# Optimization experiments

Measured on AMD Instinct MI355X. Metric: run time of the kernel, lower is better.

Reference implementation:

```python
import jax, jax.numpy as jnp
import numpy as np

B, T, V, WD = 32, 2048, 50000, 300        # batch, max_doc_len, batch vocab, word_dim
P, L, ND = 150, 7, 2                      # total patterns, max_pattern_length, num_diags
BIAS_SCALE = 1.0
ZERO = -100.0                             # max-plus semiring zero (repo: neg_infinity = -100*ones)
# end state per pattern = pattern_length - 1, for pattern_specs {5:50, 6:50, 7:50}
END_STATES = np.concatenate([np.full(50, 4), np.full(50, 5), np.full(50, 6)]).astype(np.int32)


def setup_inputs() -> dict:
    key = jax.random.key(0)
    ks = jax.random.split(key, 10)
    diags = jax.random.normal(ks[0], (P * ND * L, WD), jnp.float32)
    diags = diags / jnp.linalg.norm(diags, axis=1, keepdims=True)  # normalize() in __init__
    return {
        "embeddings_matrix": jax.random.normal(ks[1], (WD, V), jnp.float32),
        "diags": diags,
        "bias": jax.random.normal(ks[2], (P * ND * L, 1), jnp.float32),
        "epsilon": jax.random.normal(ks[3], (P, L - 1), jnp.float32),
        "mlp_w0": jax.random.normal(ks[4], (P, 100), jnp.float32) * 0.1,
        "mlp_b0": jnp.zeros((100,), jnp.float32),
        "mlp_w1": jax.random.normal(ks[5], (100, 2), jnp.float32) * 0.1,
        "mlp_b1": jnp.zeros((2,), jnp.float32),
        "docs": jax.random.randint(ks[6], (B, T), 0, V),
        "doc_lens": jax.random.randint(ks[7], (B,), 5, T + 1),
    }


def reference(embeddings_matrix, diags, bias, epsilon, mlp_w0, mlp_b0, mlp_w1, mlp_b1, docs, doc_lens):
    # Max-plus semiring: from_float = identity, times = +, plus = max, one = 0, zero = -100.
    # Transition scores for every token in the batch vocabulary: [V, P*ND*L]
    trans = (diags @ embeddings_matrix + BIAS_SCALE * bias).T
    # Gather per doc token, reshape, time-major: [T, B, P, ND, L]
    tm = trans[docs].reshape(B, T, P, ND, L).transpose(1, 0, 2, 3, 4)

    end_states = jnp.asarray(END_STATES)               # [P]
    active = jnp.arange(T)[:, None] < doc_lens[None, :]  # [T, B]

    zero_pad = jnp.full((B, P, 1), ZERO, trans.dtype)
    restart_pad = jnp.zeros((B, P, 1), trans.dtype)      # semiring one
    hid0 = jnp.full((B, P, L), ZERO, trans.dtype).at[:, :, 0].set(0.0)
    scores0 = jnp.full((B, P), ZERO, trans.dtype)
    eps_val = epsilon                                    # epsilon_scale = semiring one (=0) -> identity

    def step(carry, xs):
        hid, sc = carry
        tmat, act = xs  # tmat: [B, P, ND, L], act: [B]
        # epsilon transitions (shift by one state, additive in max-plus)
        after_eps = jnp.maximum(hid, jnp.concatenate([zero_pad, hid[:, :, :-1] + eps_val], axis=2))
        # main-path transitions (diag index -1), with restart padding at state 0
        main = jnp.concatenate([restart_pad, after_eps[:, :, :-1] + tmat[:, :, -1, :-1]], axis=2)
        # self loops (diag index 0); self_loop_scale = semiring one = 0
        self_loop = hid + tmat[:, :, 0, :]
        hid = jnp.maximum(main, self_loop)
        end_vals = jnp.take_along_axis(hid, end_states[None, :, None], axis=2)[:, :, 0]  # [B, P]
        sc = jnp.where(act[:, None], jnp.maximum(sc, end_vals), sc)
        return (hid, sc), None

    (_, scores), _ = jax.lax.scan(step, (hid0, scores0), (tm, active))
    # MLP head: Linear -> relu -> Linear
    h = scores @ mlp_w0 + mlp_b0
    return jax.nn.relu(h) @ mlp_w1 + mlp_b1
```

## Files before the change

kernel.cpp:

```cpp
#include <hip/hip_runtime.h>
#include <stdint.h>

#define B_   32
#define T_   2048
#define V_   50000
#define WD_  300
#define P_   150
#define KP   320
#define MP   2112
#define MB2  2176
#define NPAD 50048
#define CHUNK 64
#define NCH   32
#define NEGC (-1.0e30f)
#define VT_  391
#define MT_  17
#define NWG  6647

#define WS_EMBT      0u
#define WS_DIAGSB    32030720u
#define WS_TRANS     33423360u
#define WS_CHUNKOUT  0u
#define WS_NEEDED    244623360u

typedef __attribute__((ext_vector_type(8))) short bf16x8;
typedef __attribute__((ext_vector_type(4))) float f32x4;

#define GLOAD_LDS16(gp, lp) __builtin_amdgcn_global_load_lds( \
    (__attribute__((address_space(1))) void*)(gp), \
    (__attribute__((address_space(3))) void*)(lp), 16, 0, 0)

__device__ __forceinline__ unsigned short f2bf(float f){
  unsigned u = __builtin_bit_cast(unsigned, f);
  u = u + 0x7fffu + ((u >> 16) & 1u);
  return (unsigned short)(u >> 16);
}
__device__ __forceinline__ float bf_lo(unsigned u){ return __builtin_bit_cast(float, u << 16); }
__device__ __forceinline__ float bf_hi(unsigned u){ return __builtin_bit_cast(float, u & 0xffff0000u); }

__global__ __launch_bounds__(256) void k_transpose_emb(const float* __restrict__ emb,
                                                       unsigned short* __restrict__ embT){
  __shared__ float tile[32][65];
  int v0 = blockIdx.x * 64, k0 = blockIdx.y * 32;
  int tid = threadIdx.x;
  #pragma unroll
  for (int it = 0; it < 8; ++it){
    int idx = it * 256 + tid;
    int kk = idx >> 6, vv = idx & 63;
    int k = k0 + kk, v = v0 + vv;
    float val = 0.f;
    if (k < WD_ && v < V_) val = emb[(size_t)k * V_ + v];
    tile[kk][vv] = val;
  }
  __syncthreads();
  int row = tid >> 2, c = tid & 3;
  unsigned short e[8];
  #pragma unroll
  for (int i = 0; i < 8; ++i) e[i] = f2bf(tile[c*8 + i][row]);
  uint4 pk;
  pk.x = (unsigned)e[0] | ((unsigned)e[1] << 16);
  pk.y = (unsigned)e[2] | ((unsigned)e[3] << 16);
  pk.z = (unsigned)e[4] | ((unsigned)e[5] << 16);
  pk.w = (unsigned)e[6] | ((unsigned)e[7] << 16);
  *(uint4*)&embT[(size_t)(v0 + row) * KP + k0 + c*8] = pk;
}

__global__ __launch_bounds__(256) void k_conv_diags(const float* __restrict__ diags,
                                                    unsigned short* __restrict__ diagsB){
  int gid = blockIdx.x * 256 + threadIdx.x;
  int m = gid / 80;
  int k4 = (gid % 80) * 4;
  unsigned short e[4];
  #pragma unroll
  for (int i = 0; i < 4; ++i){
    int k = k4 + i;
    float v = (m < 2100 && k < WD_) ? diags[m * WD_ + k] : 0.f;
    e[i] = f2bf(v);
  }
  uint2 pk;
  pk.x = (unsigned)e[0] | ((unsigned)e[1] << 16);
  pk.y = (unsigned)e[2] | ((unsigned)e[3] << 16);
  *(uint2*)&diagsB[(size_t)m * KP + k4] = pk;
}

__global__ __launch_bounds__(256, 4) void k_gemm(const unsigned short* __restrict__ embT,
                                                 const unsigned short* __restrict__ diagsB,
                                                 const float* __restrict__ bias,
                                                 unsigned short* __restrict__ trans){
  __shared__ char smem[33792];
  int orig = blockIdx.x;
  int xcd = orig & 7, bidx = orig >> 3;
  int wg = (xcd < 7 ? xcd * 831 : 5817 + (xcd - 7) * 830) + bidx;
  int vt = wg / MT_, mt = wg - vt * MT_;
  int v0 = vt * 128, m0 = mt * 128;

  int tid = threadIdx.x;
  int w = tid >> 6, l = tid & 63;
  int wv = w & 1, wm = w >> 1;
  int lrow = l & 15, lq = l >> 4;

  f32x4 acc[4][4];
  #pragma unroll
  for (int i = 0; i < 4; ++i)
    #pragma unroll
    for (int j = 0; j < 4; ++j)
      acc[i][j] = (f32x4){0.f, 0.f, 0.f, 0.f};

  auto STAGE = [&](int buf, int kt){
    int k0 = kt * 32;
    char* bA = smem + buf * 16384;
    char* bB = bA + 8192;
    #pragma unroll
    for (int it = 0; it < 2; ++it){
      int idx = it * 256 + tid;
      int row = idx >> 2, slot = idx & 3;
      int sc = slot ^ ((row >> 1) & 3);
      GLOAD_LDS16(&embT[(size_t)(v0 + row) * KP + k0 + sc * 8], bA + idx * 16);
      GLOAD_LDS16(&diagsB[(size_t)(m0 + row) * KP + k0 + sc * 8], bB + idx * 16);
    }
  };

  STAGE(0, 0);
  #pragma unroll
  for (int kt = 0; kt < 10; ++kt){
    if (kt < 9){
      STAGE((kt + 1) & 1, kt + 1);
      asm volatile("s_waitcnt vmcnt(4)" ::: "memory");
    } else {
      asm volatile("s_waitcnt vmcnt(0)" ::: "memory");
    }
    __builtin_amdgcn_s_barrier();
    __builtin_amdgcn_sched_barrier(0);
    char* bA = smem + (kt & 1) * 16384;
    char* bB = bA + 8192;
    bf16x8 af[4], bg[4];
    #pragma unroll
    for (int i = 0; i < 4; ++i){
      int row = wv * 64 + i * 16 + lrow;
      af[i] = *(const bf16x8*)(bA + row * 64 + (lq ^ ((row >> 1) & 3)) * 16);
    }
    #pragma unroll
    for (int j = 0; j < 4; ++j){
      int row = wm * 64 + j * 16 + lrow;
      bg[j] = *(const bf16x8*)(bB + row * 64 + (lq ^ ((row >> 1) & 3)) * 16);
    }
    #pragma unroll
    for (int i = 0; i < 4; ++i)
      #pragma unroll
      for (int j = 0; j < 4; ++j)
        acc[i][j] = __builtin_amdgcn_mfma_f32_16x16x32_bf16(af[i], bg[j], acc[i][j], 0, 0, 0);
    __builtin_amdgcn_sched_barrier(0);
    __builtin_amdgcn_s_barrier();
  }

  float bv4[4];
  #pragma unroll
  for (int j = 0; j < 4; ++j){
    int mg = m0 + wm * 64 + j * 16 + lrow;
    bv4[j] = (mg < 2100) ? bias[mg] : 0.f;
  }
  unsigned short* eb = (unsigned short*)smem;
  #pragma unroll
  for (int i = 0; i < 4; ++i)
    #pragma unroll
    for (int j = 0; j < 4; ++j)
      #pragma unroll
      for (int r = 0; r < 4; ++r){
        int row = wv * 64 + i * 16 + lq * 4 + r;
        int col = wm * 64 + j * 16 + lrow;
        eb[row * 132 + col] = f2bf(acc[i][j][r] + bv4[j]);
      }
  __syncthreads();
  #pragma unroll
  for (int it = 0; it < 16; ++it){
    int idx2 = it * 256 + tid;
    int row = idx2 >> 5, ch = idx2 & 31;
    int vg = v0 + row, mg = m0 + ch * 4;
    if (vg < V_ && mg < MP){
      uint2 val = *(const uint2*)(smem + row * 264 + ch * 8);
      *(uint2*)&trans[(size_t)vg * MP + mg] = val;
    }
  }
}

__global__ __launch_bounds__(192) void k_scan(const unsigned short* __restrict__ trans,
                                              const int* __restrict__ docs,
                                              const int* __restrict__ doc_lens,
                                              const float* __restrict__ epsilon,
                                              float* __restrict__ chunkout){
  __shared__ int sdocs[CHUNK];
  int b = blockIdx.x >> 5, ch = blockIdx.x & 31;
  int tid = threadIdx.x;
  if (tid < CHUNK) sdocs[tid] = docs[b * T_ + ch * CHUNK + tid];
  __syncthreads();
  int p = tid;
  if (p >= P_) return;
  int doclen = doc_lens[b];
  float eps_r[6];
  #pragma unroll
  for (int i = 0; i < 6; ++i) eps_r[i] = epsilon[p*6 + i];
  int endsel = p / 50;

  float col[7][7], bvec[7], uvec[7], w;
  #pragma unroll
  for (int j = 0; j < 7; ++j)
    #pragma unroll
    for (int l = 0; l < 7; ++l) col[j][l] = (j == l) ? 0.f : NEGC;
  #pragma unroll
  for (int l = 0; l < 7; ++l){ bvec[l] = NEGC; uvec[l] = NEGC; }
  w = NEGC;

  const char* transB = (const char*)trans;

  auto LOADQ = [&](unsigned* q, int s){
    int idx = s < 63 ? s : 63;
    const unsigned* rp = (const unsigned*)(transB + (size_t)sdocs[idx] * (MP*2) + p*28);
    #pragma unroll
    for (int i = 0; i < 7; ++i) q[i] = rp[i];
  };

  auto step = [&](const unsigned* q, bool act){
    float tsf[7], tmn[6];
    tsf[0]=bf_lo(q[0]); tsf[1]=bf_hi(q[0]);
    tsf[2]=bf_lo(q[1]); tsf[3]=bf_hi(q[1]);
    tsf[4]=bf_lo(q[2]); tsf[5]=bf_hi(q[2]);
    tsf[6]=bf_lo(q[3]); tmn[0]=bf_hi(q[3]);
    tmn[1]=bf_lo(q[4]); tmn[2]=bf_hi(q[4]);
    tmn[3]=bf_lo(q[5]); tmn[4]=bf_hi(q[5]);
    tmn[5]=bf_lo(q[6]);
    #pragma unroll
    for (int j = 0; j < 7; ++j){
      #pragma unroll
      for (int l = 6; l >= 1; --l){
        if (l < j) continue;
        if (l == j){ col[j][l] = col[j][l] + tsf[l]; continue; }
        float ae;
        if (l - 1 == j) ae = col[j][l-1];
        else ae = fmaxf(col[j][l-1], col[j][l-2] + eps_r[l-2]);
        col[j][l] = fmaxf(ae + tmn[l-1], col[j][l] + tsf[l]);
      }
      if (j == 0) col[0][0] += tsf[0];
    }
    #pragma unroll
    for (int l = 6; l >= 1; --l){
      float ae;
      if (l == 1) ae = fmaxf(bvec[0], -100.0f);
      else ae = fmaxf(bvec[l-1], bvec[l-2] + eps_r[l-2]);
      bvec[l] = fmaxf(ae + tmn[l-1], bvec[l] + tsf[l]);
    }
    bvec[0] = fmaxf(0.0f, bvec[0] + tsf[0]);
    if (act){
      #pragma unroll
      for (int j = 0; j < 7; ++j){
        float c4 = (j <= 4) ? col[j][4] : NEGC;
        float c5 = (j <= 5) ? col[j][5] : NEGC;
        float c6 = col[j][6];
        float ce = (endsel == 0) ? c4 : ((endsel == 1) ? c5 : c6);
        uvec[j] = fmaxf(uvec[j], ce);
      }
      float be = (endsel == 0) ? bvec[4] : ((endsel == 1) ? bvec[5] : bvec[6]);
      w = fmaxf(w, be);
    }
  };

  unsigned q0[7], q1[7], q2[7], q3[7];
  LOADQ(q0, 0); LOADQ(q1, 1); LOADQ(q2, 2);
  int tbase = ch * CHUNK;
  for (int s = 0; s < CHUNK; s += 4){
    LOADQ(q3, s + 3); step(q0, (tbase + s)     < doclen);
    LOADQ(q0, s + 4); step(q1, (tbase + s + 1) < doclen);
    LOADQ(q1, s + 5); step(q2, (tbase + s + 2) < doclen);
    LOADQ(q2, s + 6); step(q3, (tbase + s + 3) < doclen);
  }

  float out[44];
  int idx = 0;
  #pragma unroll
  for (int j = 0; j < 7; ++j)
    #pragma unroll
    for (int l = j; l < 7; ++l) out[idx++] = col[j][l];
  #pragma unroll
  for (int l = 0; l < 7; ++l) out[28 + l] = bvec[l];
  #pragma unroll
  for (int l = 0; l < 7; ++l) out[35 + l] = uvec[l];
  out[42] = w; out[43] = 0.f;
  float* dst = chunkout + ((size_t)(b * NCH + ch) * P_ + p) * 44;
  #pragma unroll
  for (int i = 0; i < 11; ++i){
    float4 t2 = make_float4(out[4*i], out[4*i+1], out[4*i+2], out[4*i+3]);
    ((float4*)dst)[i] = t2;
  }
}

__global__ __launch_bounds__(192) void k_combine_mlp(const float* __restrict__ chunkout,
                                                     const float* __restrict__ w0,
                                                     const float* __restrict__ b0,
                                                     const float* __restrict__ w1,
                                                     const float* __restrict__ b1,
                                                     float* __restrict__ out){
  __shared__ float ssc[P_];
  __shared__ float sh[100];
  int b = blockIdx.x, tid = threadIdx.x;
  if (tid < P_){
    int p = tid;
    float h[7] = {0.f, -100.f, -100.f, -100.f, -100.f, -100.f, -100.f};
    float sc = -100.f;
    for (int ch = 0; ch < NCH; ++ch){
      const float* rec = chunkout + ((size_t)(b * NCH + ch) * P_ + p) * 44;
      float r[44];
      #pragma unroll
      for (int i = 0; i < 11; ++i){
        float4 t = ((const float4*)rec)[i];
        r[4*i] = t.x; r[4*i+1] = t.y; r[4*i+2] = t.z; r[4*i+3] = t.w;
      }
      #pragma unroll
      for (int j = 0; j < 7; ++j) sc = fmaxf(sc, r[35 + j] + h[j]);
      sc = fmaxf(sc, r[42]);
      constexpr int off[7] = {0, 7, 13, 18, 22, 25, 27};
      float nh[7];
      #pragma unroll
      for (int l = 0; l < 7; ++l){
        float v = r[28 + l];
        #pragma unroll
        for (int j = 0; j < 7; ++j){
          if (j <= l) v = fmaxf(v, r[off[j] + (l - j)] + h[j]);
        }
        nh[l] = v;
      }
      #pragma unroll
      for (int l = 0; l < 7; ++l) h[l] = nh[l];
    }
    ssc[p] = sc;
  }
  __syncthreads();
  if (tid < 100){
    float a = b0[tid];
    for (int pp = 0; pp < P_; ++pp) a += ssc[pp] * w0[pp * 100 + tid];
    sh[tid] = fmaxf(a, 0.f);
  }
  __syncthreads();
  if (tid < 2){
    float o = b1[tid];
    for (int j = 0; j < 100; ++j) o += sh[j] * w1[j * 2 + tid];
    out[b * 2 + tid] = o;
  }
}

extern "C" void kernel_launch(void* const* d_in, const int* in_sizes, int n_in,
                              void* d_out, int out_size, void* d_ws, size_t ws_size,
                              hipStream_t stream){
  const float* emb   = (const float*)d_in[0];
  const float* diags = (const float*)d_in[1];
  const float* bias  = (const float*)d_in[2];
  const float* eps   = (const float*)d_in[3];
  const float* w0    = (const float*)d_in[4];
  const float* b0    = (const float*)d_in[5];
  const float* w1    = (const float*)d_in[6];
  const float* b1    = (const float*)d_in[7];
  const int* docs    = (const int*)d_in[8];
  const int* dlens   = (const int*)d_in[9];

  if (ws_size < (size_t)WS_NEEDED) return;

  char* ws = (char*)d_ws;
  unsigned short* embT   = (unsigned short*)(ws + WS_EMBT);
  unsigned short* diagsB = (unsigned short*)(ws + WS_DIAGSB);
  unsigned short* trans  = (unsigned short*)(ws + WS_TRANS);
  float* chunkout        = (float*)(ws + WS_CHUNKOUT);
  float* outp = (float*)d_out;

  k_transpose_emb<<<dim3(NPAD/64, KP/32), 256, 0, stream>>>(emb, embT);
  k_conv_diags<<<(MB2*80 + 255)/256, 256, 0, stream>>>(diags, diagsB);
  k_gemm<<<NWG, 256, 0, stream>>>(embT, diagsB, bias, trans);
  k_scan<<<B_ * NCH, 192, 0, stream>>>(trans, docs, dlens, eps, chunkout);
  k_combine_mlp<<<B_, 192, 0, stream>>>(chunkout, w0, b0, w1, b1, outp);
}
```

Measured before the change: 220.7 us.

## Enlarge GEMM tile to 256x128, skip inactive scan chunks, use smaller chunks

The GEMM now uses 512-thread workgroups with a 256-row vocab tile, so each diags tile is reused across twice as many rows and the workgroup count is halved. The epilogue is split into two halves to fit LDS. The scan exits early for chunks entirely past doc_len, and the combine kernel stops at the last active chunk. When the workspace is large enough, 32-token chunks are used to expose more parallelism. The costs are higher register and LDS pressure per workgroup, lower occupancy, and an extra epilogue barrier.

After: 622.5 us. 182% more time.

```diff
diff --git a/kernel.cpp b/kernel.cpp
--- a/kernel.cpp
+++ b/kernel.cpp
@@ -9,19 +9,17 @@
 #define KP   320
 #define MP   2112
 #define MB2  2176
-#define NPAD 50048
-#define CHUNK 64
-#define NCH   32
+#define NPAD2 50176
+#define VT2  196
+#define MT_  17
+#define NWG2 3332
 #define NEGC (-1.0e30f)
-#define VT_  391
-#define MT_  17
-#define NWG  6647
-
-#define WS_EMBT      0u
-#define WS_DIAGSB    32030720u
-#define WS_TRANS     33423360u
-#define WS_CHUNKOUT  0u
-#define WS_NEEDED    244623360u
+
+#define WS_DIAGSB      32112640u
+#define WS_TRANS_BIG   54067200u
+#define WS_TRANS_SMALL 33505280u
+#define WS_NEED_BIG    265267200u
+#define WS_NEED_SMALL  244705280u
 
 typedef __attribute__((ext_vector_type(8))) short bf16x8;
 typedef __attribute__((ext_vector_type(4))) float f32x4;
@@ -83,20 +81,20 @@
   *(uint2*)&diagsB[(size_t)m * KP + k4] = pk;
 }
 
-__global__ __launch_bounds__(256, 4) void k_gemm(const unsigned short* __restrict__ embT,
+__global__ __launch_bounds__(512, 6) void k_gemm(const unsigned short* __restrict__ embT,
                                                  const unsigned short* __restrict__ diagsB,
                                                  const float* __restrict__ bias,
                                                  unsigned short* __restrict__ trans){
-  __shared__ char smem[33792];
+  __shared__ char smem[49152];
   int orig = blockIdx.x;
   int xcd = orig & 7, bidx = orig >> 3;
-  int wg = (xcd < 7 ? xcd * 831 : 5817 + (xcd - 7) * 830) + bidx;
+  int wg = (xcd < 4 ? xcd * 417 : 1668 + (xcd - 4) * 416) + bidx;
   int vt = wg / MT_, mt = wg - vt * MT_;
-  int v0 = vt * 128, m0 = mt * 128;
+  int v0 = vt * 256, m0 = mt * 128;
 
   int tid = threadIdx.x;
   int w = tid >> 6, l = tid & 63;
-  int wv = w & 1, wm = w >> 1;
+  int wm = w & 1, wv = w >> 1;
   int lrow = l & 15, lq = l >> 4;
 
   f32x4 acc[4][4];
@@ -108,15 +106,19 @@
 
   auto STAGE = [&](int buf, int kt){
     int k0 = kt * 32;
-    char* bA = smem + buf * 16384;
-    char* bB = bA + 8192;
+    char* bA = smem + buf * 24576;
+    char* bB = bA + 16384;
     #pragma unroll
     for (int it = 0; it < 2; ++it){
-      int idx = it * 256 + tid;
+      int idx = it * 512 + tid;
       int row = idx >> 2, slot = idx & 3;
       int sc = slot ^ ((row >> 1) & 3);
       GLOAD_LDS16(&embT[(size_t)(v0 + row) * KP + k0 + sc * 8], bA + idx * 16);
-      GLOAD_LDS16(&diagsB[(size_t)(m0 + row) * KP + k0 + sc * 8], bB + idx * 16);
+    }
+    {
+      int row = tid >> 2, slot = tid & 3;
+      int sc = slot ^ ((row >> 1) & 3);
+      GLOAD_LDS16(&diagsB[(size_t)(m0 + row) * KP + k0 + sc * 8], bB + tid * 16);
     }
   };
 
@@ -125,14 +127,14 @@
   for (int kt = 0; kt < 10; ++kt){
     if (kt < 9){
       STAGE((kt + 1) & 1, kt + 1);
-      asm volatile("s_waitcnt vmcnt(4)" ::: "memory");
+      asm volatile("s_waitcnt vmcnt(3)" ::: "memory");
     } else {
       asm volatile("s_waitcnt vmcnt(0)" ::: "memory");
     }
     __builtin_amdgcn_s_barrier();
     __builtin_amdgcn_sched_barrier(0);
-    char* bA = smem + (kt & 1) * 16384;
-    char* bB = bA + 8192;
+    char* bA = smem + (kt & 1) * 24576;
+    char* bB = bA + 16384;
     bf16x8 af[4], bg[4];
     #pragma unroll
     for (int i = 0; i < 4; ++i){
@@ -161,41 +163,51 @@
   }
   unsigned short* eb = (unsigned short*)smem;
   #pragma unroll
-  for (int i = 0; i < 4; ++i)
-    #pragma unroll
-    for (int j = 0; j < 4; ++j)
-      #pragma unroll
-      for (int r = 0; r < 4; ++r){
-        int row = wv * 64 + i * 16 + lq * 4 + r;
-        int col = wm * 64 + j * 16 + lrow;
-        eb[row * 132 + col] = f2bf(acc[i][j][r] + bv4[j]);
-      }
-  __syncthreads();
-  #pragma unroll
-  for (int it = 0; it < 16; ++it){
-    int idx2 = it * 256 + tid;
-    int row = idx2 >> 5, ch = idx2 & 31;
-    int vg = v0 + row, mg = m0 + ch * 4;
-    if (vg < V_ && mg < MP){
-      uint2 val = *(const uint2*)(smem + row * 264 + ch * 8);
-      *(uint2*)&trans[(size_t)vg * MP + mg] = val;
-    }
-  }
-}
-
+  for (int h = 0; h < 2; ++h){
+    if (h) __syncthreads();
+    if ((wv >> 1) == h){
+      #pragma unroll
+      for (int i = 0; i < 4; ++i)
+        #pragma unroll
+        for (int j = 0; j < 4; ++j)
+          #pragma unroll
+          for (int r = 0; r < 4; ++r){
+            int row = (wv & 1) * 64 + i * 16 + lq * 4 + r;
+            int col = wm * 64 + j * 16 + lrow;
+            eb[row * 132 + col] = f2bf(acc[i][j][r] + bv4[j]);
+          }
+    }
+    __syncthreads();
+    #pragma unroll
+    for (int it = 0; it < 8; ++it){
+      int idx2 = it * 512 + tid;
+      int row = idx2 >> 5, chq = idx2 & 31;
+      int vg = v0 + h * 128 + row, mg = m0 + chq * 4;
+      if (vg < V_ && mg < MP){
+        uint2 val = *(const uint2*)(smem + row * 264 + chq * 8);
+        *(uint2*)&trans[(size_t)vg * MP + mg] = val;
+      }
+    }
+  }
+}
+
+template<int CH>
 __global__ __launch_bounds__(192) void k_scan(const unsigned short* __restrict__ trans,
                                               const int* __restrict__ docs,
                                               const int* __restrict__ doc_lens,
                                               const float* __restrict__ epsilon,
                                               float* __restrict__ chunkout){
-  __shared__ int sdocs[CHUNK];
-  int b = blockIdx.x >> 5, ch = blockIdx.x & 31;
+  constexpr int NCHT = T_ / CH;
+  __shared__ int sdocs[CH];
+  int b = blockIdx.x / NCHT, ch = blockIdx.x % NCHT;
+  int doclen = doc_lens[b];
+  int tbase = ch * CH;
+  if (tbase >= doclen) return;
   int tid = threadIdx.x;
-  if (tid < CHUNK) sdocs[tid] = docs[b * T_ + ch * CHUNK + tid];
+  if (tid < CH) sdocs[tid] = docs[b * T_ + tbase + tid];
   __syncthreads();
   int p = tid;
   if (p >= P_) return;
-  int doclen = doc_lens[b];
   float eps_r[6];
   #pragma unroll
   for (int i = 0; i < 6; ++i) eps_r[i] = epsilon[p*6 + i];
@@ -213,7 +225,7 @@
   const char* transB = (const char*)trans;
 
   auto LOADQ = [&](unsigned* q, int s){
-    int idx = s < 63 ? s : 63;
+    int idx = s < CH - 1 ? s : CH - 1;
     const unsigned* rp = (const unsigned*)(transB + (size_t)sdocs[idx] * (MP*2) + p*28);
     #pragma unroll
     for (int i = 0; i < 7; ++i) q[i] = rp[i];
@@ -265,8 +277,7 @@
 
   unsigned q0[7], q1[7], q2[7], q3[7];
   LOADQ(q0, 0); LOADQ(q1, 1); LOADQ(q2, 2);
-  int tbase = ch * CHUNK;
-  for (int s = 0; s < CHUNK; s += 4){
+  for (int s = 0; s < CH; s += 4){
     LOADQ(q3, s + 3); step(q0, (tbase + s)     < doclen);
     LOADQ(q0, s + 4); step(q1, (tbase + s + 1) < doclen);
     LOADQ(q1, s + 5); step(q2, (tbase + s + 2) < doclen);
@@ -284,7 +295,7 @@
   #pragma unroll
   for (int l = 0; l < 7; ++l) out[35 + l] = uvec[l];
   out[42] = w; out[43] = 0.f;
-  float* dst = chunkout + ((size_t)(b * NCH + ch) * P_ + p) * 44;
+  float* dst = chunkout + ((size_t)(b * NCHT + ch) * P_ + p) * 44;
   #pragma unroll
   for (int i = 0; i < 11; ++i){
     float4 t2 = make_float4(out[4*i], out[4*i+1], out[4*i+2], out[4*i+3]);
@@ -293,20 +304,25 @@
 }
 
 __global__ __launch_bounds__(192) void k_combine_mlp(const float* __restrict__ chunkout,
+                                                     const int* __restrict__ doc_lens,
                                                      const float* __restrict__ w0,
                                                      const float* __restrict__ b0,
                                                      const float* __restrict__ w1,
                                                      const float* __restrict__ b1,
-                                                     float* __restrict__ out){
+                                                     float* __restrict__ out,
+                                                     int nch, int chsz){
   __shared__ float ssc[P_];
   __shared__ float sh[100];
   int b = blockIdx.x, tid = threadIdx.x;
   if (tid < P_){
     int p = tid;
+    int doclen = doc_lens[b];
+    int nact = (doclen + chsz - 1) / chsz;
+    if (nact > nch) nact = nch;
     float h[7] = {0.f, -100.f, -100.f, -100.f, -100.f, -100.f, -100.f};
     float sc = -100.f;
-    for (int ch = 0; ch < NCH; ++ch){
-      const float* rec = chunkout + ((size_t)(b * NCH + ch) * P_ + p) * 44;
+    for (int ch = 0; ch < nact; ++ch){
+      const float* rec = chunkout + ((size_t)(b * nch + ch) * P_ + p) * 44;
       float r[44];
       #pragma unroll
       for (int i = 0; i < 11; ++i){
@@ -360,18 +376,24 @@
   const int* docs    = (const int*)d_in[8];
   const int* dlens   = (const int*)d_in[9];
 
-  if (ws_size < (size_t)WS_NEEDED) return;
+  if (ws_size < (size_t)WS_NEED_SMALL) return;
+  bool big = ws_size >= (size_t)WS_NEED_BIG;
 
   char* ws = (char*)d_ws;
-  unsigned short* embT   = (unsigned short*)(ws + WS_EMBT);
+  unsigned short* embT   = (unsigned short*)(ws);
   unsigned short* diagsB = (unsigned short*)(ws + WS_DIAGSB);
-  unsigned short* trans  = (unsigned short*)(ws + WS_TRANS);
-  float* chunkout        = (float*)(ws + WS_CHUNKOUT);
+  unsigned short* trans  = (unsigned short*)(ws + (big ? WS_TRANS_BIG : WS_TRANS_SMALL));
+  float* chunkout        = (float*)(ws);
   float* outp = (float*)d_out;
 
-  k_transpose_emb<<<dim3(NPAD/64, KP/32), 256, 0, stream>>>(emb, embT);
+  k_transpose_emb<<<dim3(NPAD2/64, KP/32), 256, 0, stream>>>(emb, embT);
   k_conv_diags<<<(MB2*80 + 255)/256, 256, 0, stream>>>(diags, diagsB);
-  k_gemm<<<NWG, 256, 0, stream>>>(embT, diagsB, bias, trans);
-  k_scan<<<B_ * NCH, 192, 0, stream>>>(trans, docs, dlens, eps, chunkout);
-  k_combine_mlp<<<B_, 192, 0, stream>>>(chunkout, w0, b0, w1, b1, outp);
-}
+  k_gemm<<<NWG2, 512, 0, stream>>>(embT, diagsB, bias, trans);
+  if (big){
+    k_scan<32><<<B_ * 64, 192, 0, stream>>>(trans, docs, dlens, eps, chunkout);
+    k_combine_mlp<<<B_, 192, 0, stream>>>(chunkout, dlens, w0, b0, w1, b1, outp, 64, 32);
+  } else {
+    k_scan<64><<<B_ * 32, 192, 0, stream>>>(trans, docs, dlens, eps, chunkout);
+    k_combine_mlp<<<B_, 192, 0, stream>>>(chunkout, dlens, w0, b0, w1, b1, outp, 32, 64);
+  }
+}
```
